# Performance work log

Hardware: AMD Instinct MI355X
Metric: run time of the kernel (lower is better)

Reference implementation:

```python
import jax, jax.numpy as jnp
import numpy as np

B, N, C = 2, 2048, 2048
H, KV = 16, 4          # query heads, kv heads
D = C // H             # head_dim = 128
ROPE_BASE = 10000.0


def rope_cos_sin(position_ids, dim):
    # interleaved RoPE: freqs for even indices, repeated pairwise to full dim
    inv_freq = 1.0 / (ROPE_BASE ** (jnp.arange(0, dim, 2, dtype=jnp.float32) / dim))
    ang = position_ids[..., None].astype(jnp.float32) * inv_freq   # [B, N, D/2]
    cos = jnp.repeat(jnp.cos(ang), 2, axis=-1)                     # [B, N, D]
    sin = jnp.repeat(jnp.sin(ang), 2, axis=-1)
    return cos, sin


def rotate_half_interleaved(x):
    # (x0, x1, x2, x3, ...) -> (-x1, x0, -x3, x2, ...)
    x1 = x[..., 0::2]
    x2 = x[..., 1::2]
    return jnp.stack([-x2, x1], axis=-1).reshape(x.shape)


def apply_rotary(x, cos, sin):
    # x: [B, h, N, D]; cos/sin: [B, N, D]
    return x * cos[:, None] + rotate_half_interleaved(x) * sin[:, None]


def setup_inputs() -> dict:
    key = jax.random.key(0)
    ks = jax.random.split(key, 5)
    s = 0.02
    return dict(
        x=jax.random.normal(ks[0], (B, N, C), jnp.float32),
        position_ids=jnp.tile(jnp.arange(N, dtype=jnp.int32), (B, 1)),
        Wq=jax.random.normal(ks[1], (C, C), jnp.float32) * s,
        bq=jnp.zeros((C,), jnp.float32),
        Wk=jax.random.normal(ks[2], (C, KV * D), jnp.float32) * s,
        bk=jnp.zeros((KV * D,), jnp.float32),
        Wv=jax.random.normal(ks[3], (C, KV * D), jnp.float32) * s,
        bv=jnp.zeros((KV * D,), jnp.float32),
        Wo=jax.random.normal(ks[4], (C, C), jnp.float32) * s,
    )


def reference(x, position_ids, Wq, bq, Wk, bk, Wv, bv, Wo):
    Bx, Nx, Cx = x.shape
    q = (x @ Wq + bq).reshape(Bx, Nx, H, D).transpose(0, 2, 1, 3)   # [B,H,N,D]
    k = (x @ Wk + bk).reshape(Bx, Nx, KV, D).transpose(0, 2, 1, 3)  # [B,KV,N,D]
    v = (x @ Wv + bv).reshape(Bx, Nx, KV, D).transpose(0, 2, 1, 3)

    cos, sin = rope_cos_sin(position_ids, D)
    q = apply_rotary(q, cos, sin)
    k = apply_rotary(k, cos, sin)

    # GQA expand: head h uses kv head h // groups (matches unsqueeze+expand+reshape)
    groups = H // KV
    k = jnp.repeat(k, groups, axis=1)   # [B,H,N,D]
    v = jnp.repeat(v, groups, axis=1)

    attn = jnp.einsum('bhqd,bhkd->bhqk', q, k) * (D ** -0.5)        # [B,H,N,N]
    causal_mask = jnp.triu(jnp.ones((Nx, Nx), dtype=bool), 1)
    attn = jnp.where(causal_mask, -jnp.inf, attn)
    attn = jax.nn.softmax(attn, axis=-1)

    out = jnp.einsum('bhqk,bhkd->bhqd', attn, v)
    out = out.transpose(0, 2, 1, 3).reshape(Bx, Nx, Cx)
    return out @ Wo
```

## Files before the change

### kernel.cpp

```cpp
#include <hip/hip_runtime.h>
#include <cstdint>
#include <type_traits>

typedef unsigned short u16;
typedef unsigned int u32;
typedef __bf16 bf16x8 __attribute__((ext_vector_type(8)));
typedef short s16x8 __attribute__((ext_vector_type(8)));
typedef float f32x4 __attribute__((ext_vector_type(4)));

constexpr int BB = 2;
constexpr int SEQ = 2048;
constexpr int CH = 2048;
constexpr int NH = 16;
constexpr int NKV = 4;
constexpr int HD = 128;
constexpr int QKVC = CH + 2 * NKV * HD;

#define DI __device__ __forceinline__

DI u16 f2b(float x) {
  u32 u = __float_as_uint(x);
  u = u + 0x7FFFu + ((u >> 16) & 1u);
  return (u16)(u >> 16);
}
DI float b2f(u16 u) { return __uint_as_float(((u32)u) << 16); }

DI void glds16(const void* g, void* l) {
  __builtin_amdgcn_global_load_lds(
      (__attribute__((address_space(1))) void*)(uintptr_t)g,
      (__attribute__((address_space(3))) void*)(u32)(uintptr_t)l, 16, 0, 0);
}

__global__ __launch_bounds__(256) void xconv_kernel(const float* __restrict__ in,
                                                    u16* __restrict__ out, int n4) {
  int i = blockIdx.x * 256 + threadIdx.x;
  if (i < n4) {
    float4 v = *(const float4*)&in[(size_t)i * 4];
    ushort4 o;
    o.x = f2b(v.x); o.y = f2b(v.y); o.z = f2b(v.z); o.w = f2b(v.w);
    *(ushort4*)&out[(size_t)i * 4] = o;
  }
}

__global__ __launch_bounds__(256) void wtrans4_kernel(
    const float* __restrict__ Wq, const float* __restrict__ Wk,
    const float* __restrict__ Wv, const float* __restrict__ Wo,
    u16* __restrict__ wqkvt, u16* __restrict__ wot) {
  const int z = blockIdx.z;
  const float* in;
  u16* out;
  int Cc;
  if (z == 0)      { in = Wq; out = wqkvt;                                Cc = CH; }
  else if (z == 1) { in = Wk; out = wqkvt + (size_t)CH * CH;              Cc = NKV * HD; }
  else if (z == 2) { in = Wv; out = wqkvt + (size_t)(CH + NKV * HD) * CH; Cc = NKV * HD; }
  else             { in = Wo; out = wot;                                  Cc = CH; }
  if ((int)blockIdx.y * 64 >= Cc) return;

  __shared__ u16 tile[64 * 65];
  const int r0 = blockIdx.x * 64, c0 = blockIdx.y * 64;
  const int tid = threadIdx.x;
  for (int c = tid; c < 1024; c += 256) {
    int r = c >> 4, col = (c & 15) * 4;
    float4 v = *(const float4*)&in[(size_t)(r0 + r) * Cc + c0 + col];
    tile[r * 65 + col + 0] = f2b(v.x);
    tile[r * 65 + col + 1] = f2b(v.y);
    tile[r * 65 + col + 2] = f2b(v.z);
    tile[r * 65 + col + 3] = f2b(v.w);
  }
  __syncthreads();
  for (int c = tid; c < 1024; c += 256) {
    int r = c >> 4, col = (c & 15) * 4;
    ushort4 v;
    v.x = tile[(col + 0) * 65 + r];
    v.y = tile[(col + 1) * 65 + r];
    v.z = tile[(col + 2) * 65 + r];
    v.w = tile[(col + 3) * 65 + r];
    *(ushort4*)&out[(size_t)(c0 + r) * CH + r0 + col] = v;
  }
}

__global__ __launch_bounds__(256) void vtrans_kernel(const u16* __restrict__ in,
                                                     u16* __restrict__ out) {
  __shared__ u16 tile[64 * 65];
  const int s = blockIdx.z, n0 = blockIdx.x * 64, d0 = blockIdx.y * 64;
  const int tid = threadIdx.x;
  const u16* ip = in + (size_t)s * SEQ * HD + (size_t)n0 * HD + d0;
  u16* op = out + (size_t)s * HD * SEQ + (size_t)d0 * SEQ + n0;
  for (int c = tid; c < 1024; c += 256) {
    int r = c >> 4, col = (c & 15) * 4;
    ushort4 v = *(const ushort4*)&ip[(size_t)r * HD + col];
    tile[r * 65 + col + 0] = v.x;
    tile[r * 65 + col + 1] = v.y;
    tile[r * 65 + col + 2] = v.z;
    tile[r * 65 + col + 3] = v.w;
  }
  __syncthreads();
  for (int c = tid; c < 1024; c += 256) {
    int r = c >> 4, col = (c & 15) * 4;
    ushort4 v;
    v.x = tile[(col + 0) * 65 + r];
    v.y = tile[(col + 1) * 65 + r];
    v.z = tile[(col + 2) * 65 + r];
    v.w = tile[(col + 3) * 65 + r];
    int u = col;
    int w = (u & 3) | (((u >> 5) & 1) << 2) | (((u >> 2) & 3) << 3) | (((u >> 4) & 1) << 5);
    int glp = (w >> 3) ^ (r & 7);
    int colp = glp * 8 + (w & 7);
    *(ushort4*)&op[(size_t)r * SEQ + colp] = v;
  }
}

template <int MODE>
__global__ __launch_bounds__(256, 3) void gemm_kernel(
    const u16* __restrict__ A, const u16* __restrict__ Bt,
    u16* __restrict__ Cb, float* __restrict__ Cf,
    const float* __restrict__ bq, const float* __restrict__ bk,
    const float* __restrict__ bv, int M, int Nn, int K) {
  __shared__ u16 As[128 * 32];
  __shared__ u16 Bs[128 * 32];
  const int tid = threadIdx.x;
  const int lane = tid & 63, wave = tid >> 6;
  const int wrow = wave >> 1, wcol = wave & 1;
  const int m0 = blockIdx.x * 128, n0 = blockIdx.y * 128;
  const int lm = lane & 15, lq = lane >> 4;
  f32x4 acc[4][4] = {};

  const u16* ag = A + (size_t)(m0 + (tid >> 2)) * K + (tid & 3) * 8;
  const u16* bg = Bt + (size_t)(n0 + (tid >> 2)) * K + (tid & 3) * 8;
  char* asb = (char*)As + wave * 1024;
  char* bsb = (char*)Bs + wave * 1024;
  const size_t rowskip = (size_t)64 * K;

  for (int k = 0; k < K; k += 32) {
    __syncthreads();
    glds16(ag + k, asb);
    glds16(ag + rowskip + k, asb + 4096);
    glds16(bg + k, bsb);
    glds16(bg + rowskip + k, bsb + 4096);
    __syncthreads();
    bf16x8 af[4], bfr[4];
#pragma unroll
    for (int i = 0; i < 4; i++)
      af[i] = *(const bf16x8*)&As[(wrow * 64 + i * 16 + lm) * 32 + lq * 8];
#pragma unroll
    for (int j = 0; j < 4; j++)
      bfr[j] = *(const bf16x8*)&Bs[(wcol * 64 + j * 16 + lm) * 32 + lq * 8];
#pragma unroll
    for (int i = 0; i < 4; i++)
#pragma unroll
      for (int j = 0; j < 4; j++)
        acc[i][j] = __builtin_amdgcn_mfma_f32_16x16x32_bf16(af[i], bfr[j], acc[i][j], 0, 0, 0);
  }

#pragma unroll
  for (int i = 0; i < 4; i++) {
    const int mg = m0 + wrow * 64 + i * 16 + lq * 4;
#pragma unroll
    for (int j = 0; j < 4; j++) {
      const int ng = n0 + wcol * 64 + j * 16 + lm;
      float bias = 0.f;
      if (MODE == 0)
        bias = (ng < CH) ? bq[ng] : (ng < CH + NKV * HD ? bk[ng - CH] : bv[ng - CH - NKV * HD]);
#pragma unroll
      for (int r = 0; r < 4; r++) {
        float v = acc[i][j][r] + bias;
        size_t off = (size_t)(mg + r) * Nn + ng;
        if (MODE == 0) Cb[off] = f2b(v);
        else           Cf[off] = v;
      }
    }
  }
}

__global__ __launch_bounds__(256) void rope_kernel(
    const u16* __restrict__ qkv, const int* __restrict__ pos,
    u16* __restrict__ Qo, u16* __restrict__ Ko, u16* __restrict__ Vn) {
  __shared__ float cs_s[64], sn_s[64];
  const int tok = blockIdx.x;
  const int b = tok >> 11, n = tok & (SEQ - 1);
  const int t = threadIdx.x;
  const u16* row = qkv + (size_t)tok * QKVC;
  const float LN1E4_64 = 0.14391156831212788f;

  if (t < 64) {
    float ang = (float)pos[tok] * expf(-(float)t * LN1E4_64);
    float sn, cs;
    sincosf(ang, &sn, &cs);
    cs_s[t] = cs;
    sn_s[t] = sn;
  }
  __syncthreads();

  for (int idx = t; idx < NH * 64; idx += 256) {
    int hh = idx >> 6, i = idx & 63;
    float cs = cs_s[i], sn = sn_s[i];
    float q0v = b2f(row[hh * 128 + 2 * i]);
    float q1v = b2f(row[hh * 128 + 2 * i + 1]);
    size_t off = ((size_t)(b * NH + hh) * SEQ + n) * HD + 2 * i;
    Qo[off] = f2b(q0v * cs - q1v * sn);
    Qo[off + 1] = f2b(q1v * cs + q0v * sn);
  }
  {
    int kh = t >> 6, i = t & 63;
    float cs = cs_s[i], sn = sn_s[i];
    float k0v = b2f(row[CH + kh * 128 + 2 * i]);
    float k1v = b2f(row[CH + kh * 128 + 2 * i + 1]);
    int d0 = 2 * i;
    int g = d0 >> 3;
    int gp = (g & 8) | ((g ^ n) & 7);
    int dp = gp * 8 + (d0 & 7);
    size_t off = ((size_t)(b * NKV + kh) * SEQ + n) * HD + dp;
    Ko[off] = f2b(k0v * cs - k1v * sn);
    Ko[off + 1] = f2b(k1v * cs + k0v * sn);
  }
  for (int idx = t; idx < NKV * HD; idx += 256) {
    int kh = idx >> 7, d = idx & 127;
    Vn[((size_t)(b * NKV + kh) * SEQ + n) * HD + d] = row[CH + NKV * HD + kh * 128 + d];
  }
}

__global__ __launch_bounds__(256, 2) void flash_kernel(
    const u16* __restrict__ Q, const u16* __restrict__ Kk,
    const u16* __restrict__ Vt, u16* __restrict__ Oo) {
  __shared__ u16 Kb[2][64 * 128];
  __shared__ u16 Vb[2][128 * 64];
  const int tid = threadIdx.x, lane = tid & 63, wave = tid >> 6;
  const int lm = lane & 15, lq = lane >> 4;
  const int p = blockIdx.x;
  const int h = blockIdx.y, b = blockIdx.z;
  const int q0A = p * 64, q0B = (31 - p) * 64;
  const int kvh = h >> 2;
  const u16* Qg = Q + (size_t)(b * NH + h) * SEQ * HD;
  const u16* Kg = Kk + (size_t)(b * NKV + kvh) * SEQ * HD;
  const u16* Vg = Vt + (size_t)(b * NKV + kvh) * HD * SEQ;

  bf16x8 qf[2][4];
#pragma unroll
  for (int qg = 0; qg < 2; qg++) {
    const int q0g = qg ? q0B : q0A;
    const u16* qrow = Qg + (size_t)(q0g + wave * 16 + lm) * HD;
#pragma unroll
    for (int kd = 0; kd < 4; kd++)
      qf[qg][kd] = *(const bf16x8*)&qrow[kd * 32 + lq * 8];
  }

  f32x4 oacc[2][8] = {};
  float rs[2] = {0.f, 0.f};
  const float SCL2 = 0.12754325f;
  const int nIter = 32 - p;

  auto stage = [&](int kv0, int bufi) {
    const char* kb = (const char*)(Kg + (size_t)kv0 * HD);
    char* kl = (char*)&Kb[bufi][0];
    const char* vbb = (const char*)(Vg + (size_t)kv0);
    char* vl = (char*)&Vb[bufi][0];
#pragma unroll
    for (int c = 0; c < 4; c++) {
      int ch = wave * 4 + c;
      glds16(kb + ch * 1024 + lane * 16, kl + ch * 1024);
      glds16(vbb + (size_t)(ch * 8 + (lane >> 3)) * (SEQ * 2) + (lane & 7) * 16,
             vl + ch * 1024);
    }
  };

  stage(0, 0);

  for (int t = 0; t < nIter; t++) {
    __syncthreads();
    if (t + 1 < nIter) stage((t + 1) * 64, (t + 1) & 1);
    const u16* Ks = &Kb[t & 1][0];
    const u16* Vs = &Vb[t & 1][0];
    const int kv0 = t * 64;
    const bool actA = (t <= p);

    auto run = [&](auto dualc) {
      constexpr bool DUAL = decltype(dualc)::value;
      f32x4 sv[2][4] = {};
#pragma unroll
      for (int nt = 0; nt < 4; nt++)
#pragma unroll
        for (int kd = 0; kd < 4; kd++) {
          int g = kd * 4 + lq;
          int gpp = (g & 8) | ((g ^ lm) & 7);
          bf16x8 kf = *(const bf16x8*)&Ks[(nt * 16 + lm) * 128 + gpp * 8];
          sv[1][nt] = __builtin_amdgcn_mfma_f32_16x16x32_bf16(kf, qf[1][kd], sv[1][nt], 0, 0, 0);
          if constexpr (DUAL)
            sv[0][nt] = __builtin_amdgcn_mfma_f32_16x16x32_bf16(kf, qf[0][kd], sv[0][nt], 0, 0, 0);
        }

      s16x8 pa[2][2];
      auto softmax = [&](int qg, int q0g) {
        const int base = q0g + wave * 16;
        if (kv0 + 63 > base) {
          const int qrow = base + lm;
#pragma unroll
          for (int nt = 0; nt < 4; nt++)
#pragma unroll
            for (int r = 0; r < 4; r++) {
              int kvg = kv0 + nt * 16 + lq * 4 + r;
              float pv = exp2f(sv[qg][nt][r] * SCL2);
              if (kvg > qrow) pv = 0.f;
              rs[qg] += pv;
              pa[qg][nt & 1][(nt >> 1) * 4 + r] = (short)f2b(pv);
            }
        } else {
#pragma unroll
          for (int nt = 0; nt < 4; nt++)
#pragma unroll
            for (int r = 0; r < 4; r++) {
              float pv = exp2f(sv[qg][nt][r] * SCL2);
              rs[qg] += pv;
              pa[qg][nt & 1][(nt >> 1) * 4 + r] = (short)f2b(pv);
            }
        }
      };
      softmax(1, q0B);
      if constexpr (DUAL) softmax(0, q0A);

#pragma unroll
      for (int ks = 0; ks < 2; ks++) {
        const int glp = (ks * 4 + lq) ^ (lm & 7);
#pragma unroll
        for (int dt = 0; dt < 8; dt++) {
          bf16x8 vf = *(const bf16x8*)&Vs[(dt * 16 + lm) * 64 + glp * 8];
          oacc[1][dt] = __builtin_amdgcn_mfma_f32_16x16x32_bf16(
              *(bf16x8*)&pa[1][ks], vf, oacc[1][dt], 0, 0, 0);
          if constexpr (DUAL)
            oacc[0][dt] = __builtin_amdgcn_mfma_f32_16x16x32_bf16(
                *(bf16x8*)&pa[0][ks], vf, oacc[0][dt], 0, 0, 0);
        }
      }
    };
    if (actA) run(std::integral_constant<bool, true>{});
    else      run(std::integral_constant<bool, false>{});
  }

  u16* orow = Oo + (size_t)b * SEQ * CH + (size_t)h * HD;
#pragma unroll
  for (int qg = 0; qg < 2; qg++) {
    const int q0g = qg ? q0B : q0A;
    float r0 = rs[qg];
    r0 += __shfl_xor(r0, 16);
    r0 += __shfl_xor(r0, 32);
    float inv[4];
#pragma unroll
    for (int r = 0; r < 4; r++) inv[r] = 1.0f / __shfl(r0, lq * 4 + r);
    const int qrow_base = q0g + wave * 16 + lq * 4;
#pragma unroll
    for (int dt = 0; dt < 8; dt++)
#pragma unroll
      for (int r = 0; r < 4; r++)
        orow[(size_t)(qrow_base + r) * CH + dt * 16 + lm] = f2b(oacc[qg][dt][r] * inv[r]);
  }
}

extern "C" void kernel_launch(void* const* d_in, const int* in_sizes, int n_in,
                              void* d_out, int out_size, void* d_ws, size_t ws_size,
                              hipStream_t stream) {
  const float* x = (const float*)d_in[0];
  const int* pos = (const int*)d_in[1];
  const float* Wq = (const float*)d_in[2];
  const float* bq = (const float*)d_in[3];
  const float* Wk = (const float*)d_in[4];
  const float* bk = (const float*)d_in[5];
  const float* Wv = (const float*)d_in[6];
  const float* bv = (const float*)d_in[7];
  const float* Wo = (const float*)d_in[8];
  float* out = (float*)d_out;

  char* ws = (char*)d_ws;
  u16* xb = (u16*)ws;    ws += (size_t)BB * SEQ * CH * 2;
  u16* wqkvt = (u16*)ws; ws += (size_t)QKVC * CH * 2;
  u16* wot = (u16*)ws;   ws += (size_t)CH * CH * 2;
  u16* qkv = (u16*)ws;   ws += (size_t)BB * SEQ * QKVC * 2;
  u16* qr = (u16*)ws;    ws += (size_t)BB * NH * SEQ * HD * 2;
  u16* kr = (u16*)ws;    ws += (size_t)BB * NKV * SEQ * HD * 2;
  u16* vn = (u16*)ws;    ws += (size_t)BB * NKV * SEQ * HD * 2;
  u16* vt = (u16*)ws;    ws += (size_t)BB * NKV * SEQ * HD * 2;
  u16* ao = (u16*)ws;    ws += (size_t)BB * SEQ * CH * 2;

  xconv_kernel<<<dim3(BB * SEQ * CH / 1024), 256, 0, stream>>>(x, xb, BB * SEQ * CH / 4);
  wtrans4_kernel<<<dim3(32, 32, 4), 256, 0, stream>>>(Wq, Wk, Wv, Wo, wqkvt, wot);
  gemm_kernel<0><<<dim3(32, 24), 256, 0, stream>>>(xb, wqkvt, qkv, (float*)nullptr,
                                                   bq, bk, bv, BB * SEQ, QKVC, CH);
  rope_kernel<<<dim3(BB * SEQ), 256, 0, stream>>>(qkv, pos, qr, kr, vn);
  vtrans_kernel<<<dim3(SEQ / 64, HD / 64, BB * NKV), 256, 0, stream>>>(vn, vt);
  flash_kernel<<<dim3(16, NH, BB), 256, 0, stream>>>(qr, kr, vt, ao);
  gemm_kernel<1><<<dim3(32, 16), 256, 0, stream>>>(ao, wot, (u16*)nullptr, out,
                                                   nullptr, nullptr, nullptr, BB * SEQ, CH, CH);
}
```

Before: 321.4 us.

## Compute softmax row sums via MFMA ones-column and write V directly from QKV GEMM

```diff
diff --git a/kernel.cpp b/kernel.cpp
--- a/kernel.cpp
+++ b/kernel.cpp
@@ -5,7 +5,6 @@
 typedef unsigned short u16;
 typedef unsigned int u32;
 typedef __bf16 bf16x8 __attribute__((ext_vector_type(8)));
-typedef short s16x8 __attribute__((ext_vector_type(8)));
 typedef float f32x4 __attribute__((ext_vector_type(4)));
 
 constexpr int BB = 2;
@@ -24,6 +23,10 @@
   return (u16)(u >> 16);
 }
 DI float b2f(u16 u) { return __uint_as_float(((u32)u) << 16); }
+
+DI u32 pack2bf(float lo, float hi) {
+  return __builtin_amdgcn_perm(__float_as_uint(hi), __float_as_uint(lo), 0x07060302u);
+}
 
 DI void glds16(const void* g, void* l) {
   __builtin_amdgcn_global_load_lds(
@@ -113,7 +116,7 @@
 template <int MODE>
 __global__ __launch_bounds__(256, 3) void gemm_kernel(
     const u16* __restrict__ A, const u16* __restrict__ Bt,
-    u16* __restrict__ Cb, float* __restrict__ Cf,
+    u16* __restrict__ Cb, float* __restrict__ Cf, u16* __restrict__ Vn,
     const float* __restrict__ bq, const float* __restrict__ bk,
     const float* __restrict__ bv, int M, int Nn, int K) {
   __shared__ u16 As[128 * 32];
@@ -164,9 +167,19 @@
 #pragma unroll
       for (int r = 0; r < 4; r++) {
         float v = acc[i][j][r] + bias;
-        size_t off = (size_t)(mg + r) * Nn + ng;
-        if (MODE == 0) Cb[off] = f2b(v);
-        else           Cf[off] = v;
+        if (MODE == 0) {
+          if (ng >= CH + NKV * HD) {
+            int tok = mg + r;
+            int bidx = tok >> 11, n = tok & (SEQ - 1);
+            int vcol = ng - (CH + NKV * HD);
+            int kh = vcol >> 7, d = vcol & (HD - 1);
+            Vn[((size_t)(bidx * NKV + kh) * SEQ + n) * HD + d] = f2b(v);
+          } else {
+            Cb[(size_t)(mg + r) * Nn + ng] = f2b(v);
+          }
+        } else {
+          Cf[(size_t)(mg + r) * Nn + ng] = v;
+        }
       }
     }
   }
@@ -174,7 +187,7 @@
 
 __global__ __launch_bounds__(256) void rope_kernel(
     const u16* __restrict__ qkv, const int* __restrict__ pos,
-    u16* __restrict__ Qo, u16* __restrict__ Ko, u16* __restrict__ Vn) {
+    u16* __restrict__ Qo, u16* __restrict__ Ko) {
   __shared__ float cs_s[64], sn_s[64];
   const int tok = blockIdx.x;
   const int b = tok >> 11, n = tok & (SEQ - 1);
@@ -213,17 +226,13 @@
     Ko[off] = f2b(k0v * cs - k1v * sn);
     Ko[off + 1] = f2b(k1v * cs + k0v * sn);
   }
-  for (int idx = t; idx < NKV * HD; idx += 256) {
-    int kh = idx >> 7, d = idx & 127;
-    Vn[((size_t)(b * NKV + kh) * SEQ + n) * HD + d] = row[CH + NKV * HD + kh * 128 + d];
-  }
 }
 
 __global__ __launch_bounds__(256, 2) void flash_kernel(
     const u16* __restrict__ Q, const u16* __restrict__ Kk,
     const u16* __restrict__ Vt, u16* __restrict__ Oo) {
   __shared__ u16 Kb[2][64 * 128];
-  __shared__ u16 Vb[2][128 * 64];
+  __shared__ u16 Vb[2][144 * 64];
   const int tid = threadIdx.x, lane = tid & 63, wave = tid >> 6;
   const int lm = lane & 15, lq = lane >> 4;
   const int p = blockIdx.x;
@@ -234,6 +243,8 @@
   const u16* Kg = Kk + (size_t)(b * NKV + kvh) * SEQ * HD;
   const u16* Vg = Vt + (size_t)(b * NKV + kvh) * HD * SEQ;
 
+  if (tid < 128) Vb[tid >> 6][128 * 64 + (tid & 63)] = 0x3F80;
+
   bf16x8 qf[2][4];
 #pragma unroll
   for (int qg = 0; qg < 2; qg++) {
@@ -245,7 +256,7 @@
   }
 
   f32x4 oacc[2][8] = {};
-  float rs[2] = {0.f, 0.f};
+  f32x4 oaccS[2] = {};
   const float SCL2 = 0.12754325f;
   const int nIter = 32 - p;
 
@@ -288,30 +299,32 @@
             sv[0][nt] = __builtin_amdgcn_mfma_f32_16x16x32_bf16(kf, qf[0][kd], sv[0][nt], 0, 0, 0);
         }
 
-      s16x8 pa[2][2];
+      alignas(16) u32 pad[2][2][4];
       auto softmax = [&](int qg, int q0g) {
         const int base = q0g + wave * 16;
         if (kv0 + 63 > base) {
           const int qrow = base + lm;
 #pragma unroll
-          for (int nt = 0; nt < 4; nt++)
+          for (int nt = 0; nt < 4; nt++) {
+            float pv[4];
 #pragma unroll
             for (int r = 0; r < 4; r++) {
               int kvg = kv0 + nt * 16 + lq * 4 + r;
-              float pv = exp2f(sv[qg][nt][r] * SCL2);
-              if (kvg > qrow) pv = 0.f;
-              rs[qg] += pv;
-              pa[qg][nt & 1][(nt >> 1) * 4 + r] = (short)f2b(pv);
+              float e = exp2f(sv[qg][nt][r] * SCL2);
+              pv[r] = (kvg > qrow) ? 0.f : e;
             }
+            pad[qg][nt & 1][(nt >> 1) * 2 + 0] = pack2bf(pv[0], pv[1]);
+            pad[qg][nt & 1][(nt >> 1) * 2 + 1] = pack2bf(pv[2], pv[3]);
+          }
         } else {
 #pragma unroll
-          for (int nt = 0; nt < 4; nt++)
-#pragma unroll
-            for (int r = 0; r < 4; r++) {
-              float pv = exp2f(sv[qg][nt][r] * SCL2);
-              rs[qg] += pv;
-              pa[qg][nt & 1][(nt >> 1) * 4 + r] = (short)f2b(pv);
-            }
+          for (int nt = 0; nt < 4; nt++) {
+            float pv[4];
+#pragma unroll
+            for (int r = 0; r < 4; r++) pv[r] = exp2f(sv[qg][nt][r] * SCL2);
+            pad[qg][nt & 1][(nt >> 1) * 2 + 0] = pack2bf(pv[0], pv[1]);
+            pad[qg][nt & 1][(nt >> 1) * 2 + 1] = pack2bf(pv[2], pv[3]);
+          }
         }
       };
       softmax(1, q0B);
@@ -320,15 +333,19 @@
 #pragma unroll
       for (int ks = 0; ks < 2; ks++) {
         const int glp = (ks * 4 + lq) ^ (lm & 7);
+        const bf16x8 pa1 = *(const bf16x8*)&pad[1][ks][0];
+        const bf16x8 pa0 = *(const bf16x8*)&pad[0][ks][0];
 #pragma unroll
         for (int dt = 0; dt < 8; dt++) {
           bf16x8 vf = *(const bf16x8*)&Vs[(dt * 16 + lm) * 64 + glp * 8];
-          oacc[1][dt] = __builtin_amdgcn_mfma_f32_16x16x32_bf16(
-              *(bf16x8*)&pa[1][ks], vf, oacc[1][dt], 0, 0, 0);
+          oacc[1][dt] = __builtin_amdgcn_mfma_f32_16x16x32_bf16(pa1, vf, oacc[1][dt], 0, 0, 0);
           if constexpr (DUAL)
-            oacc[0][dt] = __builtin_amdgcn_mfma_f32_16x16x32_bf16(
-                *(bf16x8*)&pa[0][ks], vf, oacc[0][dt], 0, 0, 0);
+            oacc[0][dt] = __builtin_amdgcn_mfma_f32_16x16x32_bf16(pa0, vf, oacc[0][dt], 0, 0, 0);
         }
+        bf16x8 vf8 = *(const bf16x8*)&Vs[(128 + lm) * 64 + glp * 8];
+        oaccS[1] = __builtin_amdgcn_mfma_f32_16x16x32_bf16(pa1, vf8, oaccS[1], 0, 0, 0);
+        if constexpr (DUAL)
+          oaccS[0] = __builtin_amdgcn_mfma_f32_16x16x32_bf16(pa0, vf8, oaccS[0], 0, 0, 0);
       }
     };
     if (actA) run(std::integral_constant<bool, true>{});
@@ -339,12 +356,9 @@
 #pragma unroll
   for (int qg = 0; qg < 2; qg++) {
     const int q0g = qg ? q0B : q0A;
-    float r0 = rs[qg];
-    r0 += __shfl_xor(r0, 16);
-    r0 += __shfl_xor(r0, 32);
     float inv[4];
 #pragma unroll
-    for (int r = 0; r < 4; r++) inv[r] = 1.0f / __shfl(r0, lq * 4 + r);
+    for (int r = 0; r < 4; r++) inv[r] = 1.0f / __shfl(oaccS[qg][r], lq * 16);
     const int qrow_base = q0g + wave * 16 + lq * 4;
 #pragma unroll
     for (int dt = 0; dt < 8; dt++)
@@ -381,11 +395,11 @@
 
   xconv_kernel<<<dim3(BB * SEQ * CH / 1024), 256, 0, stream>>>(x, xb, BB * SEQ * CH / 4);
   wtrans4_kernel<<<dim3(32, 32, 4), 256, 0, stream>>>(Wq, Wk, Wv, Wo, wqkvt, wot);
-  gemm_kernel<0><<<dim3(32, 24), 256, 0, stream>>>(xb, wqkvt, qkv, (float*)nullptr,
+  gemm_kernel<0><<<dim3(32, 24), 256, 0, stream>>>(xb, wqkvt, qkv, (float*)nullptr, vn,
                                                    bq, bk, bv, BB * SEQ, QKVC, CH);
-  rope_kernel<<<dim3(BB * SEQ), 256, 0, stream>>>(qkv, pos, qr, kr, vn);
+  rope_kernel<<<dim3(BB * SEQ), 256, 0, stream>>>(qkv, pos, qr, kr);
   vtrans_kernel<<<dim3(SEQ / 64, HD / 64, BB * NKV), 256, 0, stream>>>(vn, vt);
   flash_kernel<<<dim3(16, NH, BB), 256, 0, stream>>>(qr, kr, vt, ao);
-  gemm_kernel<1><<<dim3(32, 16), 256, 0, stream>>>(ao, wot, (u16*)nullptr, out,
+  gemm_kernel<1><<<dim3(32, 16), 256, 0, stream>>>(ao, wot, (u16*)nullptr, out, nullptr,
                                                    nullptr, nullptr, nullptr, BB * SEQ, CH, CH);
 }
```

Measured after the change: 312.6 us. 1.03x faster.
